# Kernel optimization log

Measured on AMD Instinct MI355X. Metric: run time of the kernel, lower is better.

## Reference

```python
import jax, jax.numpy as jnp
import numpy as np

DIM = 256
HEADS = 8
K = 32            # patch_size
HD = DIM // HEADS # head dim = 32
SCALE = HD ** -0.5
POS_BND = 25      # int(0.8 * patch_size * dilation**0.5), dilation=1
RPE_NUM = 2 * POS_BND + 1  # 51
N = 131072        # number of octree points at this depth (multiple of K)
M = N // K        # number of patches = 4096


def setup_inputs() -> dict:
    key = jax.random.key(0)
    ks = jax.random.split(key, 8)
    def winit(k, shape, fan_in):
        return jax.random.normal(k, shape, jnp.float32) * (fan_in ** -0.5)
    q_data = jax.random.normal(ks[0], (N, DIM), jnp.float32)
    kv_data = jax.random.normal(ks[1], (N, DIM), jnp.float32)
    # relative xyz offsets within each patch, in [-POS_BND, POS_BND]
    rel_pos = jax.random.randint(ks[2], (M, K, K, 3), 0, RPE_NUM).astype(jnp.int32) - POS_BND
    mask = jnp.zeros((M, K, K), jnp.float32)  # additive patch mask (0 = keep)
    Wq = winit(ks[3], (DIM, DIM), DIM)
    bq = jnp.zeros((DIM,), jnp.float32)
    Wkv = winit(ks[4], (DIM, 2 * DIM), DIM)
    bkv = jnp.zeros((2 * DIM,), jnp.float32)
    Wo = winit(ks[5], (DIM, DIM), DIM)
    bo = jnp.zeros((DIM,), jnp.float32)
    rpe_table = jax.random.normal(ks[6], (3 * RPE_NUM, HEADS), jnp.float32) * 0.02
    return dict(q_data=q_data, kv_data=kv_data, rel_pos=rel_pos, mask=mask,
                Wq=Wq, bq=bq, Wkv=Wkv, bkv=bkv, Wo=Wo, bo=bo, rpe_table=rpe_table)


def _rpe_bias(rel_pos, rpe_table):
    # rel_pos: (M, K, K, 3) int -> bias (M, H, K, K)
    idx = jnp.clip(rel_pos, -POS_BND, POS_BND) + POS_BND + jnp.arange(3, dtype=rel_pos.dtype) * RPE_NUM
    bias = rpe_table[idx].sum(axis=3)          # (M, K, K, H)
    return bias.transpose(0, 3, 1, 2)          # (M, H, K, K)


def reference(q_data, kv_data, rel_pos, mask, Wq, bq, Wkv, bkv, Wo, bo, rpe_table):
    # patch_partition with N % K == 0 is identity; dilation D == 1.
    q = (q_data @ Wq + bq).reshape(M, K, HEADS, HD).transpose(0, 2, 1, 3)   # (M,H,K,d)
    kv = (kv_data @ Wkv + bkv).reshape(M, K, 2, HEADS, HD)
    k = kv[:, :, 0].transpose(0, 2, 1, 3)                                    # (M,H,K,d)
    v = kv[:, :, 1].transpose(0, 2, 1, 3)                                    # (M,H,K,d)
    attn = jnp.einsum('mhqd,mhkd->mhqk', q * SCALE, k)                       # (M,H,K,K)
    attn = attn + _rpe_bias(rel_pos, rpe_table) + mask[:, None]
    attn = jax.nn.softmax(attn, axis=-1)
    out = jnp.einsum('mhqk,mhkd->mhqd', attn, v)                             # (M,H,K,d)
    out = out.transpose(0, 2, 1, 3).reshape(N, DIM)                          # patch_reverse
    return out @ Wo + bo
```

## Files before the change

### kernel.cpp

```cpp
#include <hip/hip_runtime.h>
#include <hip/hip_bf16.h>

#define TPB 512

typedef _Float16 half8 __attribute__((ext_vector_type(8)));
typedef float    f32x4 __attribute__((ext_vector_type(4)));

constexpr int kDIM   = 256;
constexpr int kP     = 32;
constexpr int kPOS   = 25;
constexpr int kRPE   = 51;
constexpr float kSCALE = 0.17677669529663687f;

constexpr size_t WQ_HI  = 0;
constexpr size_t WQ_LO  = 65536;
constexpr size_t WKV_HI = 131072;
constexpr size_t WKV_LO = 262144;
constexpr size_t WO_HI  = 393216;
constexpr size_t WO_LO  = 458752;
constexpr size_t WS_NEED_BYTES = 1048576;

constexpr int ARENA_BYTES = 149632;

__global__ void pack_weights(const float* __restrict__ Wq,
                             const float* __restrict__ Wkv,
                             const float* __restrict__ Wo,
                             _Float16* __restrict__ ws)
{
    int T = blockIdx.x * 256 + threadIdx.x;
    const float* W;
    _Float16* dh;
    _Float16* dl;
    int C, i;
    if (T < 8192) {
        W = Wq;  C = 256; i = T;         dh = ws + WQ_HI;  dl = ws + WQ_LO;
    } else if (T < 24576) {
        W = Wkv; C = 512; i = T - 8192;  dh = ws + WKV_HI; dl = ws + WKV_LO;
    } else {
        W = Wo;  C = 256; i = T - 24576; dh = ws + WO_HI;  dl = ws + WO_LO;
    }
    int nt = i >> 9;
    int k0 = (i >> 6) & 7;
    int l  = i & 63;
    int kb = k0 * 32 + ((l >> 4) << 3);
    int n  = nt * 16 + (l & 15);
    half8 H, L;
    #pragma unroll
    for (int j = 0; j < 8; ++j) {
        float w = W[(size_t)(kb + j) * C + n];
        _Float16 h = (_Float16)w;
        H[j] = h;
        L[j] = (_Float16)(w - (float)h);
    }
    *reinterpret_cast<half8*>(dh + (size_t)i * 8) = H;
    *reinterpret_cast<half8*>(dl + (size_t)i * 8) = L;
}

__global__ __launch_bounds__(TPB, 2)
void octree_attn_mfma(const float* __restrict__ q_data,
                      const float* __restrict__ kv_data,
                      const int*   __restrict__ rel_pos,
                      const float* __restrict__ mask,
                      const float* __restrict__ bq,
                      const float* __restrict__ bkv,
                      const float* __restrict__ bo,
                      const float* __restrict__ rpe_table,
                      const _Float16* __restrict__ wsh,
                      float* __restrict__ out)
{
    __shared__ __align__(16) char arena[ARENA_BYTES];
    _Float16* XqF_hi  = (_Float16*)(arena);
    _Float16* XqF_lo  = (_Float16*)(arena + 16384);
    _Float16* XkvF_hi = (_Float16*)(arena + 33280);
    _Float16* XkvF_lo = (_Float16*)(arena + 49664);
    float*    Qs      = (float*)   (arena + 33280);
    float*    KVs     = (float*)   (arena + 66560);
    unsigned char* rpl8 = (unsigned char*)(arena + 132608);
    float*    msk     = (float*)   (arena + 135808);
    float*    rpe_t   = (float*)   (arena + 140416);
    float*    bql     = (float*)   (arena + 145536);
    float*    bkvl    = (float*)   (arena + 146560);
    float*    bol     = (float*)   (arena + 148608);
    _Float16* AOF_hi  = XqF_hi;
    _Float16* AOF_lo  = XqF_lo;

    const int m    = blockIdx.x;
    const int tid  = threadIdx.x;
    const int wave = tid >> 6;
    const int lane = tid & 63;

    {
        const float* qsrc = q_data  + (size_t)m * kP * kDIM;
        const float* ksrc = kv_data + (size_t)m * kP * kDIM;
        #pragma unroll
        for (int rep = 0; rep < 2; ++rep) {
            int f = tid + rep * TPB;
            int row = f >> 5;
            int b   = f & 31;
            int mt = row >> 4;
            int k0 = b >> 2;
            int kg = b & 3;
            int off = ((mt * 8 + k0) * 64 + ((kg << 4) | (row & 15))) * 8;
            float4 x0 = *reinterpret_cast<const float4*>(qsrc + f * 8);
            float4 x1 = *reinterpret_cast<const float4*>(qsrc + f * 8 + 4);
            float xs[8] = {x0.x, x0.y, x0.z, x0.w, x1.x, x1.y, x1.z, x1.w};
            half8 H, L;
            #pragma unroll
            for (int j = 0; j < 8; ++j) {
                _Float16 h = (_Float16)xs[j];
                H[j] = h;
                L[j] = (_Float16)(xs[j] - (float)h);
            }
            *reinterpret_cast<half8*>(XqF_hi + off) = H;
            *reinterpret_cast<half8*>(XqF_lo + off) = L;
            float4 y0 = *reinterpret_cast<const float4*>(ksrc + f * 8);
            float4 y1 = *reinterpret_cast<const float4*>(ksrc + f * 8 + 4);
            float ys[8] = {y0.x, y0.y, y0.z, y0.w, y1.x, y1.y, y1.z, y1.w};
            #pragma unroll
            for (int j = 0; j < 8; ++j) {
                _Float16 h = (_Float16)ys[j];
                H[j] = h;
                L[j] = (_Float16)(ys[j] - (float)h);
            }
            *reinterpret_cast<half8*>(XkvF_hi + off) = H;
            *reinterpret_cast<half8*>(XkvF_lo + off) = L;
        }
        const int4* rsrc = reinterpret_cast<const int4*>(rel_pos + (size_t)m * kP * kP * 3);
        for (int f = tid; f < 768; f += TPB) {
            int4 v = rsrc[f];
            int idx = f * 4;
            int row = idx / 96;
            int col = idx % 96;
            uchar4 pk;
            pk.x = (unsigned char)(min(max(v.x, -kPOS), kPOS) + kPOS);
            pk.y = (unsigned char)(min(max(v.y, -kPOS), kPOS) + kPOS);
            pk.z = (unsigned char)(min(max(v.z, -kPOS), kPOS) + kPOS);
            pk.w = (unsigned char)(min(max(v.w, -kPOS), kPOS) + kPOS);
            *reinterpret_cast<uchar4*>(rpl8 + row * 100 + col) = pk;
        }
        const float4* msrc = reinterpret_cast<const float4*>(mask + (size_t)m * kP * kP);
        if (tid < 256) {
            int row = tid >> 3;
            int w   = tid & 7;
            *reinterpret_cast<float4*>(&msk[row * 36 + w * 4]) = msrc[tid];
        }
        for (int i = tid; i < 3 * kRPE * 8; i += TPB) {
            int idx = i >> 3;
            int h   = i & 7;
            rpe_t[h * 160 + idx] = rpe_table[i];
        }
        if (tid < 256) { bql[tid] = bq[tid]; bol[tid] = bo[tid]; }
        if (tid < 512) { bkvl[tid] = bkv[tid]; }
    }
    __syncthreads();

    {
        const _Float16* Bh = wsh + WKV_HI;
        const _Float16* Bl = wsh + WKV_LO;
        const int nt0 = wave * 4;
        f32x4 acc[2][4];
        #pragma unroll
        for (int a = 0; a < 2; ++a) {
            #pragma unroll
            for (int b = 0; b < 4; ++b) acc[a][b] = f32x4{0.f, 0.f, 0.f, 0.f};
        }
        #pragma unroll
        for (int k0 = 0; k0 < 8; ++k0) {
            half8 a0h = *reinterpret_cast<const half8*>(XkvF_hi + (k0 * 64 + lane) * 8);
            half8 a0l = *reinterpret_cast<const half8*>(XkvF_lo + (k0 * 64 + lane) * 8);
            half8 a1h = *reinterpret_cast<const half8*>(XkvF_hi + ((8 + k0) * 64 + lane) * 8);
            half8 a1l = *reinterpret_cast<const half8*>(XkvF_lo + ((8 + k0) * 64 + lane) * 8);
            #pragma unroll
            for (int ntl = 0; ntl < 4; ++ntl) {
                int nt = nt0 + ntl;
                half8 bh = *reinterpret_cast<const half8*>(Bh + ((size_t)(nt * 8 + k0) * 64 + lane) * 8);
                half8 bl = *reinterpret_cast<const half8*>(Bl + ((size_t)(nt * 8 + k0) * 64 + lane) * 8);
                acc[0][ntl] = __builtin_amdgcn_mfma_f32_16x16x32_f16(a0h, bh, acc[0][ntl], 0, 0, 0);
                acc[0][ntl] = __builtin_amdgcn_mfma_f32_16x16x32_f16(a0l, bh, acc[0][ntl], 0, 0, 0);
                acc[0][ntl] = __builtin_amdgcn_mfma_f32_16x16x32_f16(a0h, bl, acc[0][ntl], 0, 0, 0);
                acc[1][ntl] = __builtin_amdgcn_mfma_f32_16x16x32_f16(a1h, bh, acc[1][ntl], 0, 0, 0);
                acc[1][ntl] = __builtin_amdgcn_mfma_f32_16x16x32_f16(a1l, bh, acc[1][ntl], 0, 0, 0);
                acc[1][ntl] = __builtin_amdgcn_mfma_f32_16x16x32_f16(a1h, bl, acc[1][ntl], 0, 0, 0);
            }
        }
        #pragma unroll
        for (int ntl = 0; ntl < 4; ++ntl) {
            int col = (nt0 + ntl) * 16 + (lane & 15);
            float bv = bkvl[col];
            #pragma unroll
            for (int mt = 0; mt < 2; ++mt) {
                #pragma unroll
                for (int r = 0; r < 4; ++r) {
                    int row = mt * 16 + (lane >> 4) * 4 + r;
                    KVs[row * 516 + col] = acc[mt][ntl][r] + bv;
                }
            }
        }
    }
    __syncthreads();

    {
        const _Float16* Bh = wsh + WQ_HI;
        const _Float16* Bl = wsh + WQ_LO;
        const int nt0 = wave * 2;
        f32x4 acc[2][2];
        #pragma unroll
        for (int a = 0; a < 2; ++a) {
            #pragma unroll
            for (int b = 0; b < 2; ++b) acc[a][b] = f32x4{0.f, 0.f, 0.f, 0.f};
        }
        #pragma unroll
        for (int k0 = 0; k0 < 8; ++k0) {
            half8 a0h = *reinterpret_cast<const half8*>(XqF_hi + (k0 * 64 + lane) * 8);
            half8 a0l = *reinterpret_cast<const half8*>(XqF_lo + (k0 * 64 + lane) * 8);
            half8 a1h = *reinterpret_cast<const half8*>(XqF_hi + ((8 + k0) * 64 + lane) * 8);
            half8 a1l = *reinterpret_cast<const half8*>(XqF_lo + ((8 + k0) * 64 + lane) * 8);
            #pragma unroll
            for (int ntl = 0; ntl < 2; ++ntl) {
                int nt = nt0 + ntl;
                half8 bh = *reinterpret_cast<const half8*>(Bh + ((size_t)(nt * 8 + k0) * 64 + lane) * 8);
                half8 bl = *reinterpret_cast<const half8*>(Bl + ((size_t)(nt * 8 + k0) * 64 + lane) * 8);
                acc[0][ntl] = __builtin_amdgcn_mfma_f32_16x16x32_f16(a0h, bh, acc[0][ntl], 0, 0, 0);
                acc[0][ntl] = __builtin_amdgcn_mfma_f32_16x16x32_f16(a0l, bh, acc[0][ntl], 0, 0, 0);
                acc[0][ntl] = __builtin_amdgcn_mfma_f32_16x16x32_f16(a0h, bl, acc[0][ntl], 0, 0, 0);
                acc[1][ntl] = __builtin_amdgcn_mfma_f32_16x16x32_f16(a1h, bh, acc[1][ntl], 0, 0, 0);
                acc[1][ntl] = __builtin_amdgcn_mfma_f32_16x16x32_f16(a1l, bh, acc[1][ntl], 0, 0, 0);
                acc[1][ntl] = __builtin_amdgcn_mfma_f32_16x16x32_f16(a1h, bl, acc[1][ntl], 0, 0, 0);
            }
        }
        #pragma unroll
        for (int ntl = 0; ntl < 2; ++ntl) {
            int col = (nt0 + ntl) * 16 + (lane & 15);
            float bv = bql[col];
            #pragma unroll
            for (int mt = 0; mt < 2; ++mt) {
                #pragma unroll
                for (int r = 0; r < 4; ++r) {
                    int row = mt * 16 + (lane >> 4) * 4 + r;
                    Qs[row * 260 + col] = (acc[mt][ntl][r] + bv) * kSCALE;
                }
            }
        }
    }
    __syncthreads();

    {
        const int h  = wave;
        const int ri = lane >> 3;
        const int ci = lane & 7;
        float s[4][4];
        #pragma unroll
        for (int i = 0; i < 4; ++i) {
            #pragma unroll
            for (int j = 0; j < 4; ++j) s[i][j] = 0.f;
        }

        #pragma unroll
        for (int db = 0; db < 8; ++db) {
            float4 qv[4], kv[4];
            #pragma unroll
            for (int i = 0; i < 4; ++i)
                qv[i] = *reinterpret_cast<const float4*>(&Qs[(ri + 8 * i) * 260 + h * 32 + db * 4]);
            #pragma unroll
            for (int j = 0; j < 4; ++j)
                kv[j] = *reinterpret_cast<const float4*>(&KVs[(ci + 8 * j) * 516 + h * 32 + db * 4]);
            #pragma unroll
            for (int i = 0; i < 4; ++i) {
                #pragma unroll
                for (int j = 0; j < 4; ++j) {
                    s[i][j] = fmaf(qv[i].x, kv[j].x, s[i][j]);
                    s[i][j] = fmaf(qv[i].y, kv[j].y, s[i][j]);
                    s[i][j] = fmaf(qv[i].z, kv[j].z, s[i][j]);
                    s[i][j] = fmaf(qv[i].w, kv[j].w, s[i][j]);
                }
            }
        }

        #pragma unroll
        for (int i = 0; i < 4; ++i) {
            #pragma unroll
            for (int j = 0; j < 4; ++j) {
                int r = ri + 8 * i;
                int c = ci + 8 * j;
                int base = r * 100 + c * 3;
                int p0 = rpl8[base + 0];
                int p1 = rpl8[base + 1];
                int p2 = rpl8[base + 2];
                float bias = rpe_t[h * 160 + p0]
                           + rpe_t[h * 160 + 51 + p1]
                           + rpe_t[h * 160 + 102 + p2];
                s[i][j] += bias + msk[r * 36 + c];
            }
        }

        #pragma unroll
        for (int i = 0; i < 4; ++i) {
            float mx = fmaxf(fmaxf(s[i][0], s[i][1]), fmaxf(s[i][2], s[i][3]));
            mx = fmaxf(mx, __shfl_xor(mx, 1));
            mx = fmaxf(mx, __shfl_xor(mx, 2));
            mx = fmaxf(mx, __shfl_xor(mx, 4));
            float e0 = __expf(s[i][0] - mx);
            float e1 = __expf(s[i][1] - mx);
            float e2 = __expf(s[i][2] - mx);
            float e3 = __expf(s[i][3] - mx);
            float sum = e0 + e1 + e2 + e3;
            sum += __shfl_xor(sum, 1);
            sum += __shfl_xor(sum, 2);
            sum += __shfl_xor(sum, 4);
            float inv = 1.0f / sum;
            s[i][0] = e0 * inv;
            s[i][1] = e1 * inv;
            s[i][2] = e2 * inv;
            s[i][3] = e3 * inv;
        }

        #pragma unroll
        for (int i = 0; i < 4; ++i) {
            #pragma unroll
            for (int j = 0; j < 4; ++j)
                Qs[(ri + 8 * i) * 260 + h * 32 + ci + 8 * j] = s[i][j];
        }
        __syncthreads();

        float o[4][4];
        #pragma unroll
        for (int i = 0; i < 4; ++i) {
            #pragma unroll
            for (int j = 0; j < 4; ++j) o[i][j] = 0.f;
        }
        #pragma unroll 4
        for (int c = 0; c < kP; ++c) {
            float pv[4], vv[4];
            #pragma unroll
            for (int i = 0; i < 4; ++i)
                pv[i] = Qs[(ri + 8 * i) * 260 + h * 32 + c];
            #pragma unroll
            for (int j = 0; j < 4; ++j)
                vv[j] = KVs[c * 516 + 256 + h * 32 + ci + 8 * j];
            #pragma unroll
            for (int i = 0; i < 4; ++i) {
                #pragma unroll
                for (int j = 0; j < 4; ++j)
                    o[i][j] = fmaf(pv[i], vv[j], o[i][j]);
            }
        }
        #pragma unroll
        for (int i = 0; i < 4; ++i) {
            int row = ri + 8 * i;
            int mt  = row >> 4;
            #pragma unroll
            for (int j = 0; j < 4; ++j) {
                int offv = ((mt * 8 + h) * 64 + ((j << 4) | (row & 15))) * 8 + ci;
                float val = o[i][j];
                _Float16 hh = (_Float16)val;
                AOF_hi[offv] = hh;
                AOF_lo[offv] = (_Float16)(val - (float)hh);
            }
        }
    }
    __syncthreads();

    {
        const _Float16* Bh = wsh + WO_HI;
        const _Float16* Bl = wsh + WO_LO;
        const int nt0 = wave * 2;
        f32x4 acc[2][2];
        #pragma unroll
        for (int a = 0; a < 2; ++a) {
            #pragma unroll
            for (int b = 0; b < 2; ++b) acc[a][b] = f32x4{0.f, 0.f, 0.f, 0.f};
        }
        #pragma unroll
        for (int k0 = 0; k0 < 8; ++k0) {
            half8 a0h = *reinterpret_cast<const half8*>(AOF_hi + (k0 * 64 + lane) * 8);
            half8 a0l = *reinterpret_cast<const half8*>(AOF_lo + (k0 * 64 + lane) * 8);
            half8 a1h = *reinterpret_cast<const half8*>(AOF_hi + ((8 + k0) * 64 + lane) * 8);
            half8 a1l = *reinterpret_cast<const half8*>(AOF_lo + ((8 + k0) * 64 + lane) * 8);
            #pragma unroll
            for (int ntl = 0; ntl < 2; ++ntl) {
                int nt = nt0 + ntl;
                half8 bh = *reinterpret_cast<const half8*>(Bh + ((size_t)(nt * 8 + k0) * 64 + lane) * 8);
                half8 bl = *reinterpret_cast<const half8*>(Bl + ((size_t)(nt * 8 + k0) * 64 + lane) * 8);
                acc[0][ntl] = __builtin_amdgcn_mfma_f32_16x16x32_f16(a0h, bh, acc[0][ntl], 0, 0, 0);
                acc[0][ntl] = __builtin_amdgcn_mfma_f32_16x16x32_f16(a0l, bh, acc[0][ntl], 0, 0, 0);
                acc[0][ntl] = __builtin_amdgcn_mfma_f32_16x16x32_f16(a0h, bl, acc[0][ntl], 0, 0, 0);
                acc[1][ntl] = __builtin_amdgcn_mfma_f32_16x16x32_f16(a1h, bh, acc[1][ntl], 0, 0, 0);
                acc[1][ntl] = __builtin_amdgcn_mfma_f32_16x16x32_f16(a1l, bh, acc[1][ntl], 0, 0, 0);
                acc[1][ntl] = __builtin_amdgcn_mfma_f32_16x16x32_f16(a1h, bl, acc[1][ntl], 0, 0, 0);
            }
        }
        #pragma unroll
        for (int ntl = 0; ntl < 2; ++ntl) {
            int col = (nt0 + ntl) * 16 + (lane & 15);
            float bv = bol[col];
            #pragma unroll
            for (int mt = 0; mt < 2; ++mt) {
                #pragma unroll
                for (int r = 0; r < 4; ++r) {
                    int row = mt * 16 + (lane >> 4) * 4 + r;
                    out[((size_t)(m * kP + row)) * kDIM + col] = acc[mt][ntl][r] + bv;
                }
            }
        }
    }
}

__global__ __launch_bounds__(TPB, 2)
void octree_attn_valu(const float* __restrict__ q_data,
                      const float* __restrict__ kv_data,
                      const int*   __restrict__ rel_pos,
                      const float* __restrict__ mask,
                      const float* __restrict__ Wq,  const float* __restrict__ bq,
                      const float* __restrict__ Wkv, const float* __restrict__ bkv,
                      const float* __restrict__ Wo,  const float* __restrict__ bo,
                      const float* __restrict__ rpe_table,
                      float* __restrict__ out)
{
    __shared__ float Qs [kP * 260];
    __shared__ float KVs[kP * 516];
    __shared__ float AOs[kP * 260];
    __shared__ float rpe_t[8 * 160];
    __shared__ int   rpl[kP * 100];
    __shared__ float mskl[kP * 36];

    const int m = blockIdx.x;
    const int tid = threadIdx.x;
    const int wave = tid >> 6;
    const int lane = tid & 63;

    {
        const float4* qsrc = reinterpret_cast<const float4*>(q_data  + (size_t)m * kP * kDIM);
        const float4* ksrc = reinterpret_cast<const float4*>(kv_data + (size_t)m * kP * kDIM);
        #pragma unroll
        for (int rep = 0; rep < 4; ++rep) {
            int f = tid + rep * TPB;
            int row = f >> 6;
            int c4 = (f & 63) << 2;
            *reinterpret_cast<float4*>(&Qs[row * 260 + c4]) = qsrc[f];
            *reinterpret_cast<float4*>(&AOs[row * 260 + c4]) = ksrc[f];
        }
        const int4* rsrc = reinterpret_cast<const int4*>(rel_pos + (size_t)m * kP * kP * 3);
        for (int f = tid; f < 768; f += TPB) {
            int row = f / 24;
            int w = f % 24;
            *reinterpret_cast<int4*>(&rpl[row * 100 + w * 4]) = rsrc[f];
        }
        const float4* msrc = reinterpret_cast<const float4*>(mask + (size_t)m * kP * kP);
        if (tid < 256) {
            int row = tid >> 3;
            int w = tid & 7;
            *reinterpret_cast<float4*>(&mskl[row * 36 + w * 4]) = msrc[tid];
        }
        for (int i = tid; i < 3 * kRPE * 8; i += TPB)
            rpe_t[(i & 7) * 160 + (i >> 3)] = rpe_table[i];
    }
    __syncthreads();

    float qacc[4][4];
    {
        #pragma unroll
        for (int i = 0; i < 4; ++i) {
            #pragma unroll
            for (int j = 0; j < 4; ++j) qacc[i][j] = 0.f;
        }
        const int r0 = wave * 4;
        const int c0 = lane * 4;
        #pragma unroll 4
        for (int k = 0; k < kDIM; ++k) {
            float a[4];
            #pragma unroll
            for (int i = 0; i < 4; ++i) a[i] = Qs[(r0 + i) * 260 + k];
            float b[4];
            *reinterpret_cast<float4*>(b) =
                *reinterpret_cast<const float4*>(&Wq[(size_t)k * kDIM + c0]);
            #pragma unroll
            for (int i = 0; i < 4; ++i) {
                #pragma unroll
                for (int j = 0; j < 4; ++j) qacc[i][j] = fmaf(a[i], b[j], qacc[i][j]);
            }
        }
    }
    __syncthreads();
    {
        const int r0 = wave * 4;
        const int c0 = lane * 4;
        float bv[4];
        *reinterpret_cast<float4*>(bv) = *reinterpret_cast<const float4*>(&bq[c0]);
        #pragma unroll
        for (int i = 0; i < 4; ++i) {
            float4 o;
            o.x = (qacc[i][0] + bv[0]) * kSCALE;
            o.y = (qacc[i][1] + bv[1]) * kSCALE;
            o.z = (qacc[i][2] + bv[2]) * kSCALE;
            o.w = (qacc[i][3] + bv[3]) * kSCALE;
            *reinterpret_cast<float4*>(&Qs[(r0 + i) * 260 + c0]) = o;
        }
    }
    {
        float kvacc[4][8];
        #pragma unroll
        for (int i = 0; i < 4; ++i) {
            #pragma unroll
            for (int j = 0; j < 8; ++j) kvacc[i][j] = 0.f;
        }
        const int r0 = wave * 4;
        const int c0 = lane * 8;
        #pragma unroll 2
        for (int k = 0; k < kDIM; ++k) {
            float a[4];
            #pragma unroll
            for (int i = 0; i < 4; ++i) a[i] = AOs[(r0 + i) * 260 + k];
            float b[8];
            *reinterpret_cast<float4*>(&b[0]) =
                *reinterpret_cast<const float4*>(&Wkv[(size_t)k * 512 + c0]);
            *reinterpret_cast<float4*>(&b[4]) =
                *reinterpret_cast<const float4*>(&Wkv[(size_t)k * 512 + c0 + 4]);
            #pragma unroll
            for (int i = 0; i < 4; ++i) {
                #pragma unroll
                for (int j = 0; j < 8; ++j) kvacc[i][j] = fmaf(a[i], b[j], kvacc[i][j]);
            }
        }
        float bv[8];
        *reinterpret_cast<float4*>(&bv[0]) = *reinterpret_cast<const float4*>(&bkv[c0]);
        *reinterpret_cast<float4*>(&bv[4]) = *reinterpret_cast<const float4*>(&bkv[c0 + 4]);
        #pragma unroll
        for (int i = 0; i < 4; ++i) {
            #pragma unroll
            for (int j = 0; j < 8; ++j)
                KVs[(r0 + i) * 516 + c0 + j] = kvacc[i][j] + bv[j];
        }
    }
    __syncthreads();
    {
        const int h = wave;
        const int ri = lane >> 3;
        const int ci = lane & 7;
        float s[4][4];
        #pragma unroll
        for (int i = 0; i < 4; ++i) {
            #pragma unroll
            for (int j = 0; j < 4; ++j) s[i][j] = 0.f;
        }
        #pragma unroll
        for (int db = 0; db < 8; ++db) {
            float4 qv[4], kv[4];
            #pragma unroll
            for (int i = 0; i < 4; ++i)
                qv[i] = *reinterpret_cast<const float4*>(&Qs[(ri + 8 * i) * 260 + h * 32 + db * 4]);
            #pragma unroll
            for (int j = 0; j < 4; ++j)
                kv[j] = *reinterpret_cast<const float4*>(&KVs[(ci + 8 * j) * 516 + h * 32 + db * 4]);
            #pragma unroll
            for (int i = 0; i < 4; ++i) {
                #pragma unroll
                for (int j = 0; j < 4; ++j) {
                    s[i][j] = fmaf(qv[i].x, kv[j].x, s[i][j]);
                    s[i][j] = fmaf(qv[i].y, kv[j].y, s[i][j]);
                    s[i][j] = fmaf(qv[i].z, kv[j].z, s[i][j]);
                    s[i][j] = fmaf(qv[i].w, kv[j].w, s[i][j]);
                }
            }
        }
        #pragma unroll
        for (int i = 0; i < 4; ++i) {
            #pragma unroll
            for (int j = 0; j < 4; ++j) {
                int r = ri + 8 * i;
                int c = ci + 8 * j;
                int base = r * 100 + c * 3;
                int p0 = min(max(rpl[base + 0], -kPOS), kPOS) + kPOS;
                int p1 = min(max(rpl[base + 1], -kPOS), kPOS) + kPOS + kRPE;
                int p2 = min(max(rpl[base + 2], -kPOS), kPOS) + kPOS + 2 * kRPE;
                s[i][j] += rpe_t[h * 160 + p0] + rpe_t[h * 160 + p1] + rpe_t[h * 160 + p2]
                         + mskl[r * 36 + c];
            }
        }
        #pragma unroll
        for (int i = 0; i < 4; ++i) {
            float mx = fmaxf(fmaxf(s[i][0], s[i][1]), fmaxf(s[i][2], s[i][3]));
            mx = fmaxf(mx, __shfl_xor(mx, 1));
            mx = fmaxf(mx, __shfl_xor(mx, 2));
            mx = fmaxf(mx, __shfl_xor(mx, 4));
            float e0 = __expf(s[i][0] - mx);
            float e1 = __expf(s[i][1] - mx);
            float e2 = __expf(s[i][2] - mx);
            float e3 = __expf(s[i][3] - mx);
            float sum = e0 + e1 + e2 + e3;
            sum += __shfl_xor(sum, 1);
            sum += __shfl_xor(sum, 2);
            sum += __shfl_xor(sum, 4);
            float inv = 1.0f / sum;
            s[i][0] = e0 * inv;
            s[i][1] = e1 * inv;
            s[i][2] = e2 * inv;
            s[i][3] = e3 * inv;
        }
        #pragma unroll
        for (int i = 0; i < 4; ++i) {
            #pragma unroll
            for (int j = 0; j < 4; ++j)
                Qs[(ri + 8 * i) * 260 + h * 32 + ci + 8 * j] = s[i][j];
        }
        __syncthreads();
        float o[4][4];
        #pragma unroll
        for (int i = 0; i < 4; ++i) {
            #pragma unroll
            for (int j = 0; j < 4; ++j) o[i][j] = 0.f;
        }
        #pragma unroll 4
        for (int c = 0; c < kP; ++c) {
            float pv[4], vv[4];
            #pragma unroll
            for (int i = 0; i < 4; ++i) pv[i] = Qs[(ri + 8 * i) * 260 + h * 32 + c];
            #pragma unroll
            for (int j = 0; j < 4; ++j) vv[j] = KVs[c * 516 + 256 + h * 32 + ci + 8 * j];
            #pragma unroll
            for (int i = 0; i < 4; ++i) {
                #pragma unroll
                for (int j = 0; j < 4; ++j) o[i][j] = fmaf(pv[i], vv[j], o[i][j]);
            }
        }
        #pragma unroll
        for (int i = 0; i < 4; ++i) {
            #pragma unroll
            for (int j = 0; j < 4; ++j)
                AOs[(ri + 8 * i) * 260 + h * 32 + ci + 8 * j] = o[i][j];
        }
    }
    __syncthreads();
    {
        float oacc[4][4];
        #pragma unroll
        for (int i = 0; i < 4; ++i) {
            #pragma unroll
            for (int j = 0; j < 4; ++j) oacc[i][j] = 0.f;
        }
        const int r0 = wave * 4;
        const int c0 = lane * 4;
        #pragma unroll 4
        for (int k = 0; k < kDIM; ++k) {
            float a[4];
            #pragma unroll
            for (int i = 0; i < 4; ++i) a[i] = AOs[(r0 + i) * 260 + k];
            float b[4];
            *reinterpret_cast<float4*>(b) =
                *reinterpret_cast<const float4*>(&Wo[(size_t)k * kDIM + c0]);
            #pragma unroll
            for (int i = 0; i < 4; ++i) {
                #pragma unroll
                for (int j = 0; j < 4; ++j) oacc[i][j] = fmaf(a[i], b[j], oacc[i][j]);
            }
        }
        float bv[4];
        *reinterpret_cast<float4*>(bv) = *reinterpret_cast<const float4*>(&bo[c0]);
        #pragma unroll
        for (int i = 0; i < 4; ++i) {
            float4 o;
            o.x = oacc[i][0] + bv[0];
            o.y = oacc[i][1] + bv[1];
            o.z = oacc[i][2] + bv[2];
            o.w = oacc[i][3] + bv[3];
            *reinterpret_cast<float4*>(&out[((size_t)(m * kP + r0 + i)) * kDIM + c0]) = o;
        }
    }
}

extern "C" void kernel_launch(void* const* d_in, const int* in_sizes, int n_in,
                              void* d_out, int out_size, void* d_ws, size_t ws_size,
                              hipStream_t stream)
{
    const float* q_data  = (const float*)d_in[0];
    const float* kv_data = (const float*)d_in[1];
    const int*   rel_pos = (const int*)  d_in[2];
    const float* mask    = (const float*)d_in[3];
    const float* Wq      = (const float*)d_in[4];
    const float* bq      = (const float*)d_in[5];
    const float* Wkv     = (const float*)d_in[6];
    const float* bkv     = (const float*)d_in[7];
    const float* Wo      = (const float*)d_in[8];
    const float* bo      = (const float*)d_in[9];
    const float* rpe     = (const float*)d_in[10];
    float* outp = (float*)d_out;
    const int M = in_sizes[0] / (kDIM * kP);

    if (ws_size >= WS_NEED_BYTES) {
        hipLaunchKernelGGL(pack_weights, dim3(128), dim3(256), 0, stream,
                           Wq, Wkv, Wo, (_Float16*)d_ws);
        hipLaunchKernelGGL(octree_attn_mfma, dim3(M), dim3(TPB), 0, stream,
                           q_data, kv_data, rel_pos, mask, bq, bkv, bo, rpe,
                           (const _Float16*)d_ws, outp);
    } else {
        hipLaunchKernelGGL(octree_attn_valu, dim3(M), dim3(TPB), 0, stream,
                           q_data, kv_data, rel_pos, mask, Wq, bq, Wkv, bkv, Wo, bo,
                           rpe, outp);
    }
}
```

Measured before the change: 735.9 us.

## Shrink LDS arena with fp16 K/V storage and fuse Q/KV projections for occupancy

Stores K and V in LDS as fp16 instead of fp32, drops the staged bias copies, and repacks the LDS layout so the arena shrinks from about 146KB to about 78KB. Launch bounds are raised so up to four 512-thread blocks can share a CU. The Q and KV projection MFMA loops are merged into one pass with a single barrier, and global input loads are remapped so LDS fragment stores are contiguous. The VALU fallback kernel is removed. Rounding K/V to fp16 loses some precision, and the tighter register budget may cause spills.

```diff
diff --git a/kernel.cpp b/kernel.cpp
--- a/kernel.cpp
+++ b/kernel.cpp
@@ -18,9 +18,8 @@
 constexpr size_t WKV_LO = 262144;
 constexpr size_t WO_HI  = 393216;
 constexpr size_t WO_LO  = 458752;
-constexpr size_t WS_NEED_BYTES = 1048576;
-
-constexpr int ARENA_BYTES = 149632;
+
+constexpr int ARENA_BYTES = 79872;
 
 __global__ void pack_weights(const float* __restrict__ Wq,
                              const float* __restrict__ Wkv,
@@ -56,7 +55,7 @@
     *reinterpret_cast<half8*>(dl + (size_t)i * 8) = L;
 }
 
-__global__ __launch_bounds__(TPB, 2)
+__global__ __launch_bounds__(TPB, 4)
 void octree_attn_mfma(const float* __restrict__ q_data,
                       const float* __restrict__ kv_data,
                       const int*   __restrict__ rel_pos,
@@ -71,18 +70,16 @@
     __shared__ __align__(16) char arena[ARENA_BYTES];
     _Float16* XqF_hi  = (_Float16*)(arena);
     _Float16* XqF_lo  = (_Float16*)(arena + 16384);
+    float*    Qs      = (float*)   (arena);
+    _Float16* AOF_hi  = (_Float16*)(arena);
+    _Float16* AOF_lo  = (_Float16*)(arena + 16384);
     _Float16* XkvF_hi = (_Float16*)(arena + 33280);
     _Float16* XkvF_lo = (_Float16*)(arena + 49664);
-    float*    Qs      = (float*)   (arena + 33280);
-    float*    KVs     = (float*)   (arena + 66560);
-    unsigned char* rpl8 = (unsigned char*)(arena + 132608);
-    float*    msk     = (float*)   (arena + 135808);
-    float*    rpe_t   = (float*)   (arena + 140416);
-    float*    bql     = (float*)   (arena + 145536);
-    float*    bkvl    = (float*)   (arena + 146560);
-    float*    bol     = (float*)   (arena + 148608);
-    _Float16* AOF_hi  = XqF_hi;
-    _Float16* AOF_lo  = XqF_lo;
+    _Float16* Kh      = (_Float16*)(arena + 33280);
+    _Float16* Vh      = (_Float16*)(arena + 50176);
+    unsigned char* rpl8 = (unsigned char*)(arena + 67072);
+    float*    msk     = (float*)   (arena + 70272);
+    float*    rpe_t   = (float*)   (arena + 74880);
 
     const int m    = blockIdx.x;
     const int tid  = threadIdx.x;
@@ -94,15 +91,15 @@
         const float* ksrc = kv_data + (size_t)m * kP * kDIM;
         #pragma unroll
         for (int rep = 0; rep < 2; ++rep) {
-            int f = tid + rep * TPB;
-            int row = f >> 5;
-            int b   = f & 31;
-            int mt = row >> 4;
-            int k0 = b >> 2;
-            int kg = b & 3;
-            int off = ((mt * 8 + k0) * 64 + ((kg << 4) | (row & 15))) * 8;
-            float4 x0 = *reinterpret_cast<const float4*>(qsrc + f * 8);
-            float4 x1 = *reinterpret_cast<const float4*>(qsrc + f * 8 + 4);
+            int s   = tid + rep * TPB;
+            int mt  = s >> 9;
+            int k0  = (s >> 6) & 7;
+            int l   = s & 63;
+            int row = mt * 16 + (l & 15);
+            int col = k0 * 32 + ((l >> 4) << 3);
+            const float* qp = qsrc + row * kDIM + col;
+            float4 x0 = *reinterpret_cast<const float4*>(qp);
+            float4 x1 = *reinterpret_cast<const float4*>(qp + 4);
             float xs[8] = {x0.x, x0.y, x0.z, x0.w, x1.x, x1.y, x1.z, x1.w};
             half8 H, L;
             #pragma unroll
@@ -111,10 +108,11 @@
                 H[j] = h;
                 L[j] = (_Float16)(xs[j] - (float)h);
             }
-            *reinterpret_cast<half8*>(XqF_hi + off) = H;
-            *reinterpret_cast<half8*>(XqF_lo + off) = L;
-            float4 y0 = *reinterpret_cast<const float4*>(ksrc + f * 8);
-            float4 y1 = *reinterpret_cast<const float4*>(ksrc + f * 8 + 4);
+            *reinterpret_cast<half8*>(XqF_hi + s * 8) = H;
+            *reinterpret_cast<half8*>(XqF_lo + s * 8) = L;
+            const float* kp = ksrc + row * kDIM + col;
+            float4 y0 = *reinterpret_cast<const float4*>(kp);
+            float4 y1 = *reinterpret_cast<const float4*>(kp + 4);
             float ys[8] = {y0.x, y0.y, y0.z, y0.w, y1.x, y1.y, y1.z, y1.w};
             #pragma unroll
             for (int j = 0; j < 8; ++j) {
@@ -122,8 +120,8 @@
                 H[j] = h;
                 L[j] = (_Float16)(ys[j] - (float)h);
             }
-            *reinterpret_cast<half8*>(XkvF_hi + off) = H;
-            *reinterpret_cast<half8*>(XkvF_lo + off) = L;
+            *reinterpret_cast<half8*>(XkvF_hi + s * 8) = H;
+            *reinterpret_cast<half8*>(XkvF_lo + s * 8) = L;
         }
         const int4* rsrc = reinterpret_cast<const int4*>(rel_pos + (size_t)m * kP * kP * 3);
         for (int f = tid; f < 768; f += TPB) {
@@ -147,97 +145,91 @@
         for (int i = tid; i < 3 * kRPE * 8; i += TPB) {
             int idx = i >> 3;
             int h   = i & 7;
-            rpe_t[h * 160 + idx] = rpe_table[i];
-        }
-        if (tid < 256) { bql[tid] = bq[tid]; bol[tid] = bo[tid]; }
-        if (tid < 512) { bkvl[tid] = bkv[tid]; }
+            rpe_t[h * 156 + idx] = rpe_table[i];
+        }
     }
     __syncthreads();
 
+    f32x4 akv[2][4];
+    f32x4 aq[2][2];
     {
-        const _Float16* Bh = wsh + WKV_HI;
-        const _Float16* Bl = wsh + WKV_LO;
-        const int nt0 = wave * 4;
-        f32x4 acc[2][4];
         #pragma unroll
         for (int a = 0; a < 2; ++a) {
             #pragma unroll
-            for (int b = 0; b < 4; ++b) acc[a][b] = f32x4{0.f, 0.f, 0.f, 0.f};
-        }
+            for (int b = 0; b < 4; ++b) akv[a][b] = f32x4{0.f, 0.f, 0.f, 0.f};
+            #pragma unroll
+            for (int b = 0; b < 2; ++b) aq[a][b] = f32x4{0.f, 0.f, 0.f, 0.f};
+        }
+        const _Float16* BKh = wsh + WKV_HI;
+        const _Float16* BKl = wsh + WKV_LO;
+        const _Float16* BQh = wsh + WQ_HI;
+        const _Float16* BQl = wsh + WQ_LO;
+        const int ntkv = wave * 4;
+        const int ntq  = wave * 2;
         #pragma unroll
         for (int k0 = 0; k0 < 8; ++k0) {
-            half8 a0h = *reinterpret_cast<const half8*>(XkvF_hi + (k0 * 64 + lane) * 8);
-            half8 a0l = *reinterpret_cast<const half8*>(XkvF_lo + (k0 * 64 + lane) * 8);
-            half8 a1h = *reinterpret_cast<const half8*>(XkvF_hi + ((8 + k0) * 64 + lane) * 8);
-            half8 a1l = *reinterpret_cast<const half8*>(XkvF_lo + ((8 + k0) * 64 + lane) * 8);
+            half8 kv0h = *reinterpret_cast<const half8*>(XkvF_hi + (k0 * 64 + lane) * 8);
+            half8 kv0l = *reinterpret_cast<const half8*>(XkvF_lo + (k0 * 64 + lane) * 8);
+            half8 kv1h = *reinterpret_cast<const half8*>(XkvF_hi + ((8 + k0) * 64 + lane) * 8);
+            half8 kv1l = *reinterpret_cast<const half8*>(XkvF_lo + ((8 + k0) * 64 + lane) * 8);
             #pragma unroll
             for (int ntl = 0; ntl < 4; ++ntl) {
-                int nt = nt0 + ntl;
-                half8 bh = *reinterpret_cast<const half8*>(Bh + ((size_t)(nt * 8 + k0) * 64 + lane) * 8);
-                half8 bl = *reinterpret_cast<const half8*>(Bl + ((size_t)(nt * 8 + k0) * 64 + lane) * 8);
-                acc[0][ntl] = __builtin_amdgcn_mfma_f32_16x16x32_f16(a0h, bh, acc[0][ntl], 0, 0, 0);
-                acc[0][ntl] = __builtin_amdgcn_mfma_f32_16x16x32_f16(a0l, bh, acc[0][ntl], 0, 0, 0);
-                acc[0][ntl] = __builtin_amdgcn_mfma_f32_16x16x32_f16(a0h, bl, acc[0][ntl], 0, 0, 0);
-                acc[1][ntl] = __builtin_amdgcn_mfma_f32_16x16x32_f16(a1h, bh, acc[1][ntl], 0, 0, 0);
-                acc[1][ntl] = __builtin_amdgcn_mfma_f32_16x16x32_f16(a1l, bh, acc[1][ntl], 0, 0, 0);
-                acc[1][ntl] = __builtin_amdgcn_mfma_f32_16x16x32_f16(a1h, bl, acc[1][ntl], 0, 0, 0);
-            }
-        }
+                int nt = ntkv + ntl;
+                half8 bh = *reinterpret_cast<const half8*>(BKh + ((size_t)(nt * 8 + k0) * 64 + lane) * 8);
+                half8 bl = *reinterpret_cast<const half8*>(BKl + ((size_t)(nt * 8 + k0) * 64 + lane) * 8);
+                akv[0][ntl] = __builtin_amdgcn_mfma_f32_16x16x32_f16(kv0h, bh, akv[0][ntl], 0, 0, 0);
+                akv[0][ntl] = __builtin_amdgcn_mfma_f32_16x16x32_f16(kv0l, bh, akv[0][ntl], 0, 0, 0);
+                akv[0][ntl] = __builtin_amdgcn_mfma_f32_16x16x32_f16(kv0h, bl, akv[0][ntl], 0, 0, 0);
+                akv[1][ntl] = __builtin_amdgcn_mfma_f32_16x16x32_f16(kv1h, bh, akv[1][ntl], 0, 0, 0);
+                akv[1][ntl] = __builtin_amdgcn_mfma_f32_16x16x32_f16(kv1l, bh, akv[1][ntl], 0, 0, 0);
+                akv[1][ntl] = __builtin_amdgcn_mfma_f32_16x16x32_f16(kv1h, bl, akv[1][ntl], 0, 0, 0);
+            }
+            half8 q0h = *reinterpret_cast<const half8*>(XqF_hi + (k0 * 64 + lane) * 8);
+            half8 q0l = *reinterpret_cast<const half8*>(XqF_lo + (k0 * 64 + lane) * 8);
+            half8 q1h = *reinterpret_cast<const half8*>(XqF_hi + ((8 + k0) * 64 + lane) * 8);
+            half8 q1l = *reinterpret_cast<const half8*>(XqF_lo + ((8 + k0) * 64 + lane) * 8);
+            #pragma unroll
+            for (int ntl = 0; ntl < 2; ++ntl) {
+                int nt = ntq + ntl;
+                half8 bh = *reinterpret_cast<const half8*>(BQh + ((size_t)(nt * 8 + k0) * 64 + lane) * 8);
+                half8 bl = *reinterpret_cast<const half8*>(BQl + ((size_t)(nt * 8 + k0) * 64 + lane) * 8);
+                aq[0][ntl] = __builtin_amdgcn_mfma_f32_16x16x32_f16(q0h, bh, aq[0][ntl], 0, 0, 0);
+                aq[0][ntl] = __builtin_amdgcn_mfma_f32_16x16x32_f16(q0l, bh, aq[0][ntl], 0, 0, 0);
+                aq[0][ntl] = __builtin_amdgcn_mfma_f32_16x16x32_f16(q0h, bl, aq[0][ntl], 0, 0, 0);
+                aq[1][ntl] = __builtin_amdgcn_mfma_f32_16x16x32_f16(q1h, bh, aq[1][ntl], 0, 0, 0);
+                aq[1][ntl] = __builtin_amdgcn_mfma_f32_16x16x32_f16(q1l, bh, aq[1][ntl], 0, 0, 0);
+                aq[1][ntl] = __builtin_amdgcn_mfma_f32_16x16x32_f16(q1h, bl, aq[1][ntl], 0, 0, 0);
+            }
+        }
+    }
+    __syncthreads();
+
+    {
         #pragma unroll
         for (int ntl = 0; ntl < 4; ++ntl) {
-            int col = (nt0 + ntl) * 16 + (lane & 15);
-            float bv = bkvl[col];
+            int cg = (wave * 4 + ntl) * 16 + (lane & 15);
+            float bv = bkv[cg];
             #pragma unroll
             for (int mt = 0; mt < 2; ++mt) {
                 #pragma unroll
                 for (int r = 0; r < 4; ++r) {
                     int row = mt * 16 + (lane >> 4) * 4 + r;
-                    KVs[row * 516 + col] = acc[mt][ntl][r] + bv;
+                    _Float16 v = (_Float16)(akv[mt][ntl][r] + bv);
+                    if (cg < 256) Kh[row * 264 + cg] = v;
+                    else          Vh[row * 264 + (cg - 256)] = v;
                 }
             }
         }
-    }
-    __syncthreads();
-
-    {
-        const _Float16* Bh = wsh + WQ_HI;
-        const _Float16* Bl = wsh + WQ_LO;
-        const int nt0 = wave * 2;
-        f32x4 acc[2][2];
-        #pragma unroll
-        for (int a = 0; a < 2; ++a) {
-            #pragma unroll
-            for (int b = 0; b < 2; ++b) acc[a][b] = f32x4{0.f, 0.f, 0.f, 0.f};
-        }
-        #pragma unroll
-        for (int k0 = 0; k0 < 8; ++k0) {
-            half8 a0h = *reinterpret_cast<const half8*>(XqF_hi + (k0 * 64 + lane) * 8);
-            half8 a0l = *reinterpret_cast<const half8*>(XqF_lo + (k0 * 64 + lane) * 8);
-            half8 a1h = *reinterpret_cast<const half8*>(XqF_hi + ((8 + k0) * 64 + lane) * 8);
-            half8 a1l = *reinterpret_cast<const half8*>(XqF_lo + ((8 + k0) * 64 + lane) * 8);
-            #pragma unroll
-            for (int ntl = 0; ntl < 2; ++ntl) {
-                int nt = nt0 + ntl;
-                half8 bh = *reinterpret_cast<const half8*>(Bh + ((size_t)(nt * 8 + k0) * 64 + lane) * 8);
-                half8 bl = *reinterpret_cast<const half8*>(Bl + ((size_t)(nt * 8 + k0) * 64 + lane) * 8);
-                acc[0][ntl] = __builtin_amdgcn_mfma_f32_16x16x32_f16(a0h, bh, acc[0][ntl], 0, 0, 0);
-                acc[0][ntl] = __builtin_amdgcn_mfma_f32_16x16x32_f16(a0l, bh, acc[0][ntl], 0, 0, 0);
-                acc[0][ntl] = __builtin_amdgcn_mfma_f32_16x16x32_f16(a0h, bl, acc[0][ntl], 0, 0, 0);
-                acc[1][ntl] = __builtin_amdgcn_mfma_f32_16x16x32_f16(a1h, bh, acc[1][ntl], 0, 0, 0);
-                acc[1][ntl] = __builtin_amdgcn_mfma_f32_16x16x32_f16(a1l, bh, acc[1][ntl], 0, 0, 0);
-                acc[1][ntl] = __builtin_amdgcn_mfma_f32_16x16x32_f16(a1h, bl, acc[1][ntl], 0, 0, 0);
-            }
-        }
         #pragma unroll
         for (int ntl = 0; ntl < 2; ++ntl) {
-            int col = (nt0 + ntl) * 16 + (lane & 15);
-            float bv = bql[col];
+            int col = (wave * 2 + ntl) * 16 + (lane & 15);
+            float bv = bq[col];
             #pragma unroll
             for (int mt = 0; mt < 2; ++mt) {
                 #pragma unroll
                 for (int r = 0; r < 4; ++r) {
                     int row = mt * 16 + (lane >> 4) * 4 + r;
-                    Qs[row * 260 + col] = (acc[mt][ntl][r] + bv) * kSCALE;
+                    Qs[row * 260 + col] = (aq[mt][ntl][r] + bv) * kSCALE;
                 }
             }
         }
@@ -256,22 +248,27 @@
         }
 
         #pragma unroll
-        for (int db = 0; db < 8; ++db) {
-            float4 qv[4], kv[4];
-            #pragma unroll
-            for (int i = 0; i < 4; ++i)
-                qv[i] = *reinterpret_cast<const float4*>(&Qs[(ri + 8 * i) * 260 + h * 32 + db * 4]);
-            #pragma unroll
-            for (int j = 0; j < 4; ++j)
-                kv[j] = *reinterpret_cast<const float4*>(&KVs[(ci + 8 * j) * 516 + h * 32 + db * 4]);
+        for (int db = 0; db < 4; ++db) {
+            float kf[4][8];
+            #pragma unroll
+            for (int j = 0; j < 4; ++j) {
+                half8 k8 = *reinterpret_cast<const half8*>(
+                    &Kh[(ci + 8 * j) * 264 + h * 32 + db * 8]);
+                #pragma unroll
+                for (int e = 0; e < 8; ++e) kf[j][e] = (float)k8[e];
+            }
             #pragma unroll
             for (int i = 0; i < 4; ++i) {
+                float4 qa = *reinterpret_cast<const float4*>(
+                    &Qs[(ri + 8 * i) * 260 + h * 32 + db * 8]);
+                float4 qb = *reinterpret_cast<const float4*>(
+                    &Qs[(ri + 8 * i) * 260 + h * 32 + db * 8 + 4]);
+                float qf[8] = {qa.x, qa.y, qa.z, qa.w, qb.x, qb.y, qb.z, qb.w};
                 #pragma unroll
                 for (int j = 0; j < 4; ++j) {
-                    s[i][j] = fmaf(qv[i].x, kv[j].x, s[i][j]);
-                    s[i][j] = fmaf(qv[i].y, kv[j].y, s[i][j]);
-                    s[i][j] = fmaf(qv[i].z, kv[j].z, s[i][j]);
-                    s[i][j] = fmaf(qv[i].w, kv[j].w, s[i][j]);
+                    #pragma unroll
+                    for (int e = 0; e < 8; ++e)
+                        s[i][j] = fmaf(qf[e], kf[j][e], s[i][j]);
                 }
             }
         }
@@ -286,9 +283,9 @@
                 int p0 = rpl8[base + 0];
                 int p1 = rpl8[base + 1];
                 int p2 = rpl8[base + 2];
-                float bias = rpe_t[h * 160 + p0]
-                           + rpe_t[h * 160 + 51 + p1]
-                           + rpe_t[h * 160 + 102 + p2];
+                float bias = rpe_t[h * 156 + p0]
+                           + rpe_t[h * 156 + 51 + p1]
+                           + rpe_t[h * 156 + 102 + p2];
                 s[i][j] += bias + msk[r * 36 + c];
             }
         }
@@ -336,7 +333,7 @@
                 pv[i] = Qs[(ri + 8 * i) * 260 + h * 32 + c];
             #pragma unroll
             for (int j = 0; j < 4; ++j)
-                vv[j] = KVs[c * 516 + 256 + h * 32 + ci + 8 * j];
+                vv[j] = (float)Vh[c * 264 + h * 32 + ci + 8 * j];
             #pragma unroll
             for (int i = 0; i < 4; ++i) {
                 #pragma unroll
@@ -344,6 +341,8 @@
                     o[i][j] = fmaf(pv[i], vv[j], o[i][j]);
             }
         }
+        __syncthreads();
+
         #pragma unroll
         for (int i = 0; i < 4; ++i) {
             int row = ri + 8 * i;
@@ -392,7 +391,7 @@
         #pragma unroll
         for (int ntl = 0; ntl < 2; ++ntl) {
             int col = (nt0 + ntl) * 16 + (lane & 15);
-            float bv = bol[col];
+            float bv = bo[col];
             #pragma unroll
             for (int mt = 0; mt < 2; ++mt) {
                 #pragma unroll
@@ -401,268 +400,6 @@
                     out[((size_t)(m * kP + row)) * kDIM + col] = acc[mt][ntl][r] + bv;
                 }
             }
-        }
-    }
-}
-
-__global__ __launch_bounds__(TPB, 2)
-void octree_attn_valu(const float* __restrict__ q_data,
-                      const float* __restrict__ kv_data,
-                      const int*   __restrict__ rel_pos,
-                      const float* __restrict__ mask,
-                      const float* __restrict__ Wq,  const float* __restrict__ bq,
-                      const float* __restrict__ Wkv, const float* __restrict__ bkv,
-                      const float* __restrict__ Wo,  const float* __restrict__ bo,
-                      const float* __restrict__ rpe_table,
-                      float* __restrict__ out)
-{
-    __shared__ float Qs [kP * 260];
-    __shared__ float KVs[kP * 516];
-    __shared__ float AOs[kP * 260];
-    __shared__ float rpe_t[8 * 160];
-    __shared__ int   rpl[kP * 100];
-    __shared__ float mskl[kP * 36];
-
-    const int m = blockIdx.x;
-    const int tid = threadIdx.x;
-    const int wave = tid >> 6;
-    const int lane = tid & 63;
-
-    {
-        const float4* qsrc = reinterpret_cast<const float4*>(q_data  + (size_t)m * kP * kDIM);
-        const float4* ksrc = reinterpret_cast<const float4*>(kv_data + (size_t)m * kP * kDIM);
-        #pragma unroll
-        for (int rep = 0; rep < 4; ++rep) {
-            int f = tid + rep * TPB;
-            int row = f >> 6;
-            int c4 = (f & 63) << 2;
-            *reinterpret_cast<float4*>(&Qs[row * 260 + c4]) = qsrc[f];
-            *reinterpret_cast<float4*>(&AOs[row * 260 + c4]) = ksrc[f];
-        }
-        const int4* rsrc = reinterpret_cast<const int4*>(rel_pos + (size_t)m * kP * kP * 3);
-        for (int f = tid; f < 768; f += TPB) {
-            int row = f / 24;
-            int w = f % 24;
-            *reinterpret_cast<int4*>(&rpl[row * 100 + w * 4]) = rsrc[f];
-        }
-        const float4* msrc = reinterpret_cast<const float4*>(mask + (size_t)m * kP * kP);
-        if (tid < 256) {
-            int row = tid >> 3;
-            int w = tid & 7;
-            *reinterpret_cast<float4*>(&mskl[row * 36 + w * 4]) = msrc[tid];
-        }
-        for (int i = tid; i < 3 * kRPE * 8; i += TPB)
-            rpe_t[(i & 7) * 160 + (i >> 3)] = rpe_table[i];
-    }
-    __syncthreads();
-
-    float qacc[4][4];
-    {
-        #pragma unroll
-        for (int i = 0; i < 4; ++i) {
-            #pragma unroll
-            for (int j = 0; j < 4; ++j) qacc[i][j] = 0.f;
-        }
-        const int r0 = wave * 4;
-        const int c0 = lane * 4;
-        #pragma unroll 4
-        for (int k = 0; k < kDIM; ++k) {
-            float a[4];
-            #pragma unroll
-            for (int i = 0; i < 4; ++i) a[i] = Qs[(r0 + i) * 260 + k];
-            float b[4];
-            *reinterpret_cast<float4*>(b) =
-                *reinterpret_cast<const float4*>(&Wq[(size_t)k * kDIM + c0]);
-            #pragma unroll
-            for (int i = 0; i < 4; ++i) {
-                #pragma unroll
-                for (int j = 0; j < 4; ++j) qacc[i][j] = fmaf(a[i], b[j], qacc[i][j]);
-            }
-        }
-    }
-    __syncthreads();
-    {
-        const int r0 = wave * 4;
-        const int c0 = lane * 4;
-        float bv[4];
-        *reinterpret_cast<float4*>(bv) = *reinterpret_cast<const float4*>(&bq[c0]);
-        #pragma unroll
-        for (int i = 0; i < 4; ++i) {
-            float4 o;
-            o.x = (qacc[i][0] + bv[0]) * kSCALE;
-            o.y = (qacc[i][1] + bv[1]) * kSCALE;
-            o.z = (qacc[i][2] + bv[2]) * kSCALE;
-            o.w = (qacc[i][3] + bv[3]) * kSCALE;
-            *reinterpret_cast<float4*>(&Qs[(r0 + i) * 260 + c0]) = o;
-        }
-    }
-    {
-        float kvacc[4][8];
-        #pragma unroll
-        for (int i = 0; i < 4; ++i) {
-            #pragma unroll
-            for (int j = 0; j < 8; ++j) kvacc[i][j] = 0.f;
-        }
-        const int r0 = wave * 4;
-        const int c0 = lane * 8;
-        #pragma unroll 2
-        for (int k = 0; k < kDIM; ++k) {
-            float a[4];
-            #pragma unroll
-            for (int i = 0; i < 4; ++i) a[i] = AOs[(r0 + i) * 260 + k];
-            float b[8];
-            *reinterpret_cast<float4*>(&b[0]) =
-                *reinterpret_cast<const float4*>(&Wkv[(size_t)k * 512 + c0]);
-            *reinterpret_cast<float4*>(&b[4]) =
-                *reinterpret_cast<const float4*>(&Wkv[(size_t)k * 512 + c0 + 4]);
-            #pragma unroll
-            for (int i = 0; i < 4; ++i) {
-                #pragma unroll
-                for (int j = 0; j < 8; ++j) kvacc[i][j] = fmaf(a[i], b[j], kvacc[i][j]);
-            }
-        }
-        float bv[8];
-        *reinterpret_cast<float4*>(&bv[0]) = *reinterpret_cast<const float4*>(&bkv[c0]);
-        *reinterpret_cast<float4*>(&bv[4]) = *reinterpret_cast<const float4*>(&bkv[c0 + 4]);
-        #pragma unroll
-        for (int i = 0; i < 4; ++i) {
-            #pragma unroll
-            for (int j = 0; j < 8; ++j)
-                KVs[(r0 + i) * 516 + c0 + j] = kvacc[i][j] + bv[j];
-        }
-    }
-    __syncthreads();
-    {
-        const int h = wave;
-        const int ri = lane >> 3;
-        const int ci = lane & 7;
-        float s[4][4];
-        #pragma unroll
-        for (int i = 0; i < 4; ++i) {
-            #pragma unroll
-            for (int j = 0; j < 4; ++j) s[i][j] = 0.f;
-        }
-        #pragma unroll
-        for (int db = 0; db < 8; ++db) {
-            float4 qv[4], kv[4];
-            #pragma unroll
-            for (int i = 0; i < 4; ++i)
-                qv[i] = *reinterpret_cast<const float4*>(&Qs[(ri + 8 * i) * 260 + h * 32 + db * 4]);
-            #pragma unroll
-            for (int j = 0; j < 4; ++j)
-                kv[j] = *reinterpret_cast<const float4*>(&KVs[(ci + 8 * j) * 516 + h * 32 + db * 4]);
-            #pragma unroll
-            for (int i = 0; i < 4; ++i) {
-                #pragma unroll
-                for (int j = 0; j < 4; ++j) {
-                    s[i][j] = fmaf(qv[i].x, kv[j].x, s[i][j]);
-                    s[i][j] = fmaf(qv[i].y, kv[j].y, s[i][j]);
-                    s[i][j] = fmaf(qv[i].z, kv[j].z, s[i][j]);
-                    s[i][j] = fmaf(qv[i].w, kv[j].w, s[i][j]);
-                }
-            }
-        }
-        #pragma unroll
-        for (int i = 0; i < 4; ++i) {
-            #pragma unroll
-            for (int j = 0; j < 4; ++j) {
-                int r = ri + 8 * i;
-                int c = ci + 8 * j;
-                int base = r * 100 + c * 3;
-                int p0 = min(max(rpl[base + 0], -kPOS), kPOS) + kPOS;
-                int p1 = min(max(rpl[base + 1], -kPOS), kPOS) + kPOS + kRPE;
-                int p2 = min(max(rpl[base + 2], -kPOS), kPOS) + kPOS + 2 * kRPE;
-                s[i][j] += rpe_t[h * 160 + p0] + rpe_t[h * 160 + p1] + rpe_t[h * 160 + p2]
-                         + mskl[r * 36 + c];
-            }
-        }
-        #pragma unroll
-        for (int i = 0; i < 4; ++i) {
-            float mx = fmaxf(fmaxf(s[i][0], s[i][1]), fmaxf(s[i][2], s[i][3]));
-            mx = fmaxf(mx, __shfl_xor(mx, 1));
-            mx = fmaxf(mx, __shfl_xor(mx, 2));
-            mx = fmaxf(mx, __shfl_xor(mx, 4));
-            float e0 = __expf(s[i][0] - mx);
-            float e1 = __expf(s[i][1] - mx);
-            float e2 = __expf(s[i][2] - mx);
-            float e3 = __expf(s[i][3] - mx);
-            float sum = e0 + e1 + e2 + e3;
-            sum += __shfl_xor(sum, 1);
-            sum += __shfl_xor(sum, 2);
-            sum += __shfl_xor(sum, 4);
-            float inv = 1.0f / sum;
-            s[i][0] = e0 * inv;
-            s[i][1] = e1 * inv;
-            s[i][2] = e2 * inv;
-            s[i][3] = e3 * inv;
-        }
-        #pragma unroll
-        for (int i = 0; i < 4; ++i) {
-            #pragma unroll
-            for (int j = 0; j < 4; ++j)
-                Qs[(ri + 8 * i) * 260 + h * 32 + ci + 8 * j] = s[i][j];
-        }
-        __syncthreads();
-        float o[4][4];
-        #pragma unroll
-        for (int i = 0; i < 4; ++i) {
-            #pragma unroll
-            for (int j = 0; j < 4; ++j) o[i][j] = 0.f;
-        }
-        #pragma unroll 4
-        for (int c = 0; c < kP; ++c) {
-            float pv[4], vv[4];
-            #pragma unroll
-            for (int i = 0; i < 4; ++i) pv[i] = Qs[(ri + 8 * i) * 260 + h * 32 + c];
-            #pragma unroll
-            for (int j = 0; j < 4; ++j) vv[j] = KVs[c * 516 + 256 + h * 32 + ci + 8 * j];
-            #pragma unroll
-            for (int i = 0; i < 4; ++i) {
-                #pragma unroll
-                for (int j = 0; j < 4; ++j) o[i][j] = fmaf(pv[i], vv[j], o[i][j]);
-            }
-        }
-        #pragma unroll
-        for (int i = 0; i < 4; ++i) {
-            #pragma unroll
-            for (int j = 0; j < 4; ++j)
-                AOs[(ri + 8 * i) * 260 + h * 32 + ci + 8 * j] = o[i][j];
-        }
-    }
-    __syncthreads();
-    {
-        float oacc[4][4];
-        #pragma unroll
-        for (int i = 0; i < 4; ++i) {
-            #pragma unroll
-            for (int j = 0; j < 4; ++j) oacc[i][j] = 0.f;
-        }
-        const int r0 = wave * 4;
-        const int c0 = lane * 4;
-        #pragma unroll 4
-        for (int k = 0; k < kDIM; ++k) {
-            float a[4];
-            #pragma unroll
-            for (int i = 0; i < 4; ++i) a[i] = AOs[(r0 + i) * 260 + k];
-            float b[4];
-            *reinterpret_cast<float4*>(b) =
-                *reinterpret_cast<const float4*>(&Wo[(size_t)k * kDIM + c0]);
-            #pragma unroll
-            for (int i = 0; i < 4; ++i) {
-                #pragma unroll
-                for (int j = 0; j < 4; ++j) oacc[i][j] = fmaf(a[i], b[j], oacc[i][j]);
-            }
-        }
-        float bv[4];
-        *reinterpret_cast<float4*>(bv) = *reinterpret_cast<const float4*>(&bo[c0]);
-        #pragma unroll
-        for (int i = 0; i < 4; ++i) {
-            float4 o;
-            o.x = oacc[i][0] + bv[0];
-            o.y = oacc[i][1] + bv[1];
-            o.z = oacc[i][2] + bv[2];
-            o.w = oacc[i][3] + bv[3];
-            *reinterpret_cast<float4*>(&out[((size_t)(m * kP + r0 + i)) * kDIM + c0]) = o;
         }
     }
 }
@@ -685,15 +422,9 @@
     float* outp = (float*)d_out;
     const int M = in_sizes[0] / (kDIM * kP);
 
-    if (ws_size >= WS_NEED_BYTES) {
-        hipLaunchKernelGGL(pack_weights, dim3(128), dim3(256), 0, stream,
-                           Wq, Wkv, Wo, (_Float16*)d_ws);
-        hipLaunchKernelGGL(octree_attn_mfma, dim3(M), dim3(TPB), 0, stream,
-                           q_data, kv_data, rel_pos, mask, bq, bkv, bo, rpe,
-                           (const _Float16*)d_ws, outp);
-    } else {
-        hipLaunchKernelGGL(octree_attn_valu, dim3(M), dim3(TPB), 0, stream,
-                           q_data, kv_data, rel_pos, mask, Wq, bq, Wkv, bkv, Wo, bo,
-                           rpe, outp);
-    }
+    hipLaunchKernelGGL(pack_weights, dim3(128), dim3(256), 0, stream,
+                       Wq, Wkv, Wo, (_Float16*)d_ws);
+    hipLaunchKernelGGL(octree_attn_mfma, dim3(M), dim3(TPB), 0, stream,
+                       q_data, kv_data, rel_pos, mask, bq, bkv, bo, rpe,
+                       (const _Float16*)d_ws, outp);
 }
```

After: 625.8 us. 15.0% less time.
